# Optimization experiments

Measured on AMD Instinct MI355X. Metric: run time of the kernel, lower is better.

Reference implementation:

```python
import jax, jax.numpy as jnp
import numpy as np
from jax import lax

N, C, H, W = 64, 96, 18, 32
S_IN = 320          # input_state_size
HEADS, HD = 4, 96 // 4
HID = 96            # HIDDEN_SIZE
ENC = 320           # ENC_SIZE
K = 3               # KERNEL_SIZE


def _conv(x, k, b):
    y = lax.conv_general_dilated(x, k, (1, 1), 'SAME',
                                 dimension_numbers=('NCHW', 'OIHW', 'NCHW'))
    return y + b[None, :, None, None]


def setup_inputs() -> dict:
    key = jax.random.key(0)
    ks = jax.random.split(key, 16)
    sc = 0.02
    inp = {
        'x': jax.random.normal(ks[0], (N, C, H, W), jnp.float32),
        'x_state': jax.random.normal(ks[1], (N, S_IN), jnp.float32),
        'actor_keys': jax.random.randint(ks[2], (N,), 0, N),
        'hidden_states': 0.1 * jax.random.normal(ks[3], (N, HID, H, W), jnp.float32),
        # modulation Linear(S_IN -> 2*C), bias init 0
        'W_mod': sc * jax.random.normal(ks[4], (S_IN, 2 * C), jnp.float32),
        'b_mod': jnp.zeros((2 * C,), jnp.float32),
        # FiLM attention: qkv 1x1 proj and output proj
        'W_qkv': sc * jax.random.normal(ks[5], (C, 3 * C), jnp.float32),
        'b_qkv': jnp.zeros((3 * C,), jnp.float32),
        'W_proj': sc * jax.random.normal(ks[6], (C, C), jnp.float32),
        'b_proj': jnp.zeros((C,), jnp.float32),
        # IRConv2dCell (ConvGRU-style): gates conv (2C -> 2*HID), candidate conv (2C -> HID)
        'K_zr': sc * jax.random.normal(ks[7], (2 * HID, 2 * C, K, K), jnp.float32),
        'b_zr': jnp.zeros((2 * HID,), jnp.float32),
        'K_c': sc * jax.random.normal(ks[8], (HID, 2 * C, K, K), jnp.float32),
        'b_c': jnp.zeros((HID,), jnp.float32),
        # PosConv: learned positional map + 1x1 conv to ENC
        'pos_emb': sc * jax.random.normal(ks[9], (1, HID, H, W), jnp.float32),
        'W_pos': sc * jax.random.normal(ks[10], (ENC, HID), jnp.float32),
        'b_pos': jnp.zeros((ENC,), jnp.float32),
    }
    return inp


def reference(x, x_state, actor_keys, hidden_states,
              W_mod, b_mod, W_qkv, b_qkv, W_proj, b_proj,
              K_zr, b_zr, K_c, b_c, pos_emb, W_pos, b_pos):
    HW = H * W
    # modulation -> FiLM params
    mod = x_state @ W_mod + b_mod                       # [N, 2C]
    mm, mb = jnp.split(mod, 2, axis=1)                  # [N, C] each
    # FiLM-conditioned attention over spatial positions
    xm = x * mm[:, :, None, None] + mb[:, :, None, None]  # [N,C,H,W]
    xf = xm.reshape(N, C, HW).transpose(0, 2, 1)          # [N,HW,C]
    qkv = xf @ W_qkv + b_qkv                              # [N,HW,3C]
    q, k, v = jnp.split(qkv, 3, axis=-1)
    q = q.reshape(N, HW, HEADS, HD).transpose(0, 2, 1, 3)  # [N,h,HW,hd]
    k = k.reshape(N, HW, HEADS, HD).transpose(0, 2, 1, 3)
    v = v.reshape(N, HW, HEADS, HD).transpose(0, 2, 1, 3)
    attn = jax.nn.softmax(jnp.einsum('nhqd,nhkd->nhqk', q, k) / np.sqrt(HD), axis=-1)
    o = jnp.einsum('nhqk,nhkd->nhqd', attn, v)            # [N,h,HW,hd]
    o = o.transpose(0, 2, 1, 3).reshape(N, HW, C)
    o = o @ W_proj + b_proj
    y = x + o.transpose(0, 2, 1).reshape(N, C, H, W)      # residual
    # actor-keyed recurrent conv memory cell (gather per actor key)
    h = hidden_states[actor_keys]                         # [N,HID,H,W]
    xh = jnp.concatenate([y, h], axis=1)                  # [N,2C,H,W]
    zr = _conv(xh, K_zr, b_zr)
    z, r = jnp.split(jax.nn.sigmoid(zr), 2, axis=1)
    c = jnp.tanh(_conv(jnp.concatenate([y, r * h], axis=1), K_c, b_c))
    h_new = (1.0 - z) * h + z * c                         # [N,HID,H,W]
    # pooled outputs
    x_visual = h_new.reshape(N, HID, H // 2, 2, W // 2, 2).mean(axis=(3, 5))
    e = h_new + pos_emb
    enc = jnp.einsum('nchw,oc->nohw', e, W_pos) + b_pos[None, :, None, None]
    x_visual_enc = enc.max(axis=(2, 3))                   # [N,ENC]
    return (x_visual, x_visual_enc)
```

## Files before the change

kernel.cpp:

```cpp
#include <hip/hip_runtime.h>
#include <hip/hip_bf16.h>
#include <math.h>

#define NN 64
#define CC 96
#define HH 18
#define WW 32
#define HWP 576
#define SIN 320
#define NHEADS 4
#define HDIM 24
#define HIDC 96
#define ENCC 320

#define MOD_OFF   0
#define A_OFF     12288
#define Y_OFF     (A_OFF)
#define Z_OFF     (A_OFF + 3538944)
#define RH_OFF    (A_OFF + 7077888)
#define O_OFF     (A_OFF + 10616832)
#define HN_OFF    (O_OFF)
#define PART_OFF  (O_OFF + 3538944)
#define WTZR_OFF  (PART_OFF + 163840)
#define WTC_OFF   (WTZR_OFF + 165888)

typedef __attribute__((ext_vector_type(8))) short short8;
typedef __attribute__((ext_vector_type(4))) float f32x4;
typedef __attribute__((ext_vector_type(2))) unsigned int uint2v;
#define MFMA16(a, b, c) __builtin_amdgcn_mfma_f32_16x16x32_bf16(a, b, c, 0, 0, 0)

__device__ inline unsigned short f2bf(float f) {
  __hip_bfloat16 h = __float2bfloat16(f);
  return *reinterpret_cast<unsigned short*>(&h);
}
__device__ inline unsigned int cvtpk(float lo, float hi) {
  unsigned int r;
  asm volatile("v_cvt_pk_bf16_f32 %0, %1, %2" : "=v"(r) : "v"(lo), "v"(hi));
  return r;
}
union S8U { short8 s; unsigned int u[4]; };

__global__ __launch_bounds__(192) void k_mod(const float* __restrict__ xs,
    const float* __restrict__ Wm, const float* __restrict__ bm,
    float* __restrict__ mod) {
  __shared__ float s[SIN];
  int n = blockIdx.x;
  for (int i = threadIdx.x; i < SIN; i += 192) s[i] = xs[n * SIN + i];
  __syncthreads();
  int j = threadIdx.x;
  float acc = bm[j];
  #pragma unroll 4
  for (int k = 0; k < SIN; ++k) acc = fmaf(s[k], Wm[k * 192 + j], acc);
  mod[n * 192 + j] = acc;
}

__global__ __launch_bounds__(256) void k_qkv(const float* __restrict__ x,
    const float* __restrict__ mod, const float* __restrict__ Wq,
    const float* __restrict__ bq, float* __restrict__ qkv) {
  int id = blockIdx.x;
  int n = id & 63, pt = id >> 6;
  int p0 = pt * 96;
  __shared__ __align__(16) short XT[96 * 104];
  int tid = threadIdx.x, lane = tid & 63, wid = tid >> 6;
  int wr = wid >> 1, wcn = wid & 1;
  int cl = lane & 15, kg = lane >> 4;
  #pragma unroll
  for (int w = 0; w < 9; ++w) {
    int lin = tid + 256 * w;
    int cp = lin / 48, pp = (lin % 48) * 2;
    float mA = mod[n * 192 + 2 * cp], bA = mod[n * 192 + 96 + 2 * cp];
    float mB = mod[n * 192 + 2 * cp + 1], bB = mod[n * 192 + 96 + 2 * cp + 1];
    float2 xa = *reinterpret_cast<const float2*>(
        &x[((size_t)n * CC + 2 * cp) * HWP + p0 + pp]);
    float2 xb = *reinterpret_cast<const float2*>(
        &x[((size_t)n * CC + 2 * cp + 1) * HWP + p0 + pp]);
    *reinterpret_cast<unsigned int*>(&XT[pp * 104 + 2 * cp]) =
        cvtpk(fmaf(xa.x, mA, bA), fmaf(xb.x, mB, bB));
    *reinterpret_cast<unsigned int*>(&XT[(pp + 1) * 104 + 2 * cp]) =
        cvtpk(fmaf(xa.y, mA, bA), fmaf(xb.y, mB, bB));
  }
  __syncthreads();

  f32x4 acc[3][9];
  #pragma unroll
  for (int mt = 0; mt < 3; ++mt)
    #pragma unroll
    for (int nt = 0; nt < 9; ++nt) acc[mt][nt] = (f32x4){0.f, 0.f, 0.f, 0.f};

  #pragma unroll
  for (int kc = 0; kc < 3; ++kc) {
    short8 af[3];
    #pragma unroll
    for (int mt = 0; mt < 3; ++mt) {
      int row = wr * 48 + mt * 16 + cl;
      af[mt] = *reinterpret_cast<const short8*>(
          &XT[row * 104 + kc * 32 + kg * 8]);
    }
    #pragma unroll
    for (int nt = 0; nt < 9; ++nt) {
      int j = wcn * 144 + nt * 16 + cl;
      const float* wp = Wq + (size_t)(kc * 32 + kg * 8) * 288 + j;
      S8U b;
      b.u[0] = cvtpk(wp[0], wp[288]);
      b.u[1] = cvtpk(wp[576], wp[864]);
      b.u[2] = cvtpk(wp[1152], wp[1440]);
      b.u[3] = cvtpk(wp[1728], wp[2016]);
      #pragma unroll
      for (int mt = 0; mt < 3; ++mt)
        acc[mt][nt] = MFMA16(af[mt], b.s, acc[mt][nt]);
    }
  }

  #pragma unroll
  for (int nt = 0; nt < 9; ++nt) {
    int j = wcn * 144 + nt * 16 + cl;
    float bias = bq[j];
    #pragma unroll
    for (int mt = 0; mt < 3; ++mt) {
      int pr = p0 + wr * 48 + mt * 16 + kg * 4;
      float* dst = qkv + ((size_t)n * HWP + pr) * 288 + j;
      dst[0] = acc[mt][nt][0] + bias;
      dst[288] = acc[mt][nt][1] + bias;
      dst[576] = acc[mt][nt][2] + bias;
      dst[864] = acc[mt][nt][3] + bias;
    }
  }
}

__global__ __launch_bounds__(256) void k_attn(const float* __restrict__ qkv,
                                              float* __restrict__ o) {
  int id = blockIdx.x;
  int n = id & 63, head = id >> 6;
  __shared__ __align__(16) short K_lds[576 * 40];
  __shared__ __align__(16) short VT_lds[24 * 584];
  __shared__ __align__(16) short P_lds[4 * 144 * 40];
  int tid = threadIdx.x, lane = tid & 63, wid = tid >> 6;
  int cl = lane & 15, kg = lane >> 4;
  const float* base = qkv + (size_t)n * HWP * 288;
  int qoff = head * HDIM, koff = CC + head * HDIM, voff = 2 * CC + head * HDIM;
  const float scale = 0.2041241452319315f;

  for (int p = tid; p < HWP; p += 256) {
    const float* ksrc = base + (size_t)p * 288 + koff;
    #pragma unroll
    for (int g = 0; g < 3; ++g) {
      float4 a = *(const float4*)(ksrc + g * 8);
      float4 b = *(const float4*)(ksrc + g * 8 + 4);
      S8U t;
      t.u[0] = cvtpk(a.x, a.y); t.u[1] = cvtpk(a.z, a.w);
      t.u[2] = cvtpk(b.x, b.y); t.u[3] = cvtpk(b.z, b.w);
      *reinterpret_cast<short8*>(&K_lds[p * 40 + g * 8]) = t.s;
    }
    *reinterpret_cast<short8*>(&K_lds[p * 40 + 24]) =
        (short8){0, 0, 0, 0, 0, 0, 0, 0};
    const float* vsrc = base + (size_t)p * 288 + voff;
    #pragma unroll
    for (int d = 0; d < HDIM; ++d) VT_lds[d * 584 + p] = (short)f2bf(vsrc[d]);
  }

  int qbase = wid * 144;
  short8 qf[9];
  #pragma unroll
  for (int qt = 0; qt < 9; ++qt) {
    if (kg < 3) {
      const float* qs =
          base + (size_t)(qbase + qt * 16 + cl) * 288 + qoff + kg * 8;
      float4 a = *(const float4*)qs;
      float4 b = *(const float4*)(qs + 4);
      S8U t;
      t.u[0] = cvtpk(a.x * scale, a.y * scale);
      t.u[1] = cvtpk(a.z * scale, a.w * scale);
      t.u[2] = cvtpk(b.x * scale, b.y * scale);
      t.u[3] = cvtpk(b.z * scale, b.w * scale);
      qf[qt] = t.s;
    } else {
      qf[qt] = (short8){0, 0, 0, 0, 0, 0, 0, 0};
    }
  }
  __syncthreads();

  f32x4 acc[9][2];
  float m[9], l[9];
  #pragma unroll
  for (int qt = 0; qt < 9; ++qt) {
    acc[qt][0] = (f32x4){0.f, 0.f, 0.f, 0.f};
    acc[qt][1] = (f32x4){0.f, 0.f, 0.f, 0.f};
    m[qt] = -1e30f; l[qt] = 0.f;
  }
  short* pw = P_lds + wid * 5760;
  const f32x4 z4 = (f32x4){0.f, 0.f, 0.f, 0.f};

  for (int ch = 0; ch < 18; ++ch) {
    int key0 = ch * 32;
    short8 ka0 = *reinterpret_cast<const short8*>(
        &K_lds[(key0 + cl) * 40 + kg * 8]);
    short8 ka1 = *reinterpret_cast<const short8*>(
        &K_lds[(key0 + 16 + cl) * 40 + kg * 8]);
    #pragma unroll
    for (int qt = 0; qt < 9; ++qt) {
      f32x4 s0 = MFMA16(ka0, qf[qt], z4);
      f32x4 s1 = MFMA16(ka1, qf[qt], z4);
      float mx = fmaxf(fmaxf(fmaxf(s0[0], s0[1]), fmaxf(s0[2], s0[3])),
                       fmaxf(fmaxf(s1[0], s1[1]), fmaxf(s1[2], s1[3])));
      mx = fmaxf(mx, __shfl_xor(mx, 16));
      mx = fmaxf(mx, __shfl_xor(mx, 32));
      float mn = fmaxf(m[qt], mx);
      float corr = __expf(m[qt] - mn);
      float p0 = __expf(s0[0] - mn), p1 = __expf(s0[1] - mn);
      float p2 = __expf(s0[2] - mn), p3 = __expf(s0[3] - mn);
      float p4 = __expf(s1[0] - mn), p5 = __expf(s1[1] - mn);
      float p6 = __expf(s1[2] - mn), p7 = __expf(s1[3] - mn);
      float sum = ((p0 + p1) + (p2 + p3)) + ((p4 + p5) + (p6 + p7));
      sum += __shfl_xor(sum, 16);
      sum += __shfl_xor(sum, 32);
      l[qt] = l[qt] * corr + sum;
      m[qt] = mn;
      float c0 = __shfl(corr, kg * 4 + 0);
      float c1 = __shfl(corr, kg * 4 + 1);
      float c2 = __shfl(corr, kg * 4 + 2);
      float c3 = __shfl(corr, kg * 4 + 3);
      acc[qt][0][0] *= c0; acc[qt][0][1] *= c1;
      acc[qt][0][2] *= c2; acc[qt][0][3] *= c3;
      acc[qt][1][0] *= c0; acc[qt][1][1] *= c1;
      acc[qt][1][2] *= c2; acc[qt][1][3] *= c3;
      uint2v w0 = {cvtpk(p0, p1), cvtpk(p2, p3)};
      uint2v w1 = {cvtpk(p4, p5), cvtpk(p6, p7)};
      short* prow = pw + (qt * 16 + cl) * 40;
      *reinterpret_cast<uint2v*>(&prow[4 * kg]) = w0;
      *reinterpret_cast<uint2v*>(&prow[16 + 4 * kg]) = w1;
    }
    short8 vb0 = *reinterpret_cast<const short8*>(
        &VT_lds[cl * 584 + key0 + kg * 8]);
    short8 vb1 = (cl < 8) ? *reinterpret_cast<const short8*>(
                                &VT_lds[(16 + cl) * 584 + key0 + kg * 8])
                          : (short8){0, 0, 0, 0, 0, 0, 0, 0};
    #pragma unroll
    for (int qt = 0; qt < 9; ++qt) {
      short8 pa = *reinterpret_cast<const short8*>(
          &pw[(qt * 16 + cl) * 40 + kg * 8]);
      acc[qt][0] = MFMA16(pa, vb0, acc[qt][0]);
      acc[qt][1] = MFMA16(pa, vb1, acc[qt][1]);
    }
  }

  #pragma unroll
  for (int qt = 0; qt < 9; ++qt) {
    float li0 = 1.f / __shfl(l[qt], kg * 4 + 0);
    float li1 = 1.f / __shfl(l[qt], kg * 4 + 1);
    float li2 = 1.f / __shfl(l[qt], kg * 4 + 2);
    float li3 = 1.f / __shfl(l[qt], kg * 4 + 3);
    #pragma unroll
    for (int dt = 0; dt < 2; ++dt) {
      int d = dt * 16 + cl;
      if (dt == 1 && cl >= 8) continue;
      size_t ob = ((size_t)n * HWP + qbase + qt * 16 + kg * 4) * CC
                  + head * HDIM + d;
      o[ob] = acc[qt][dt][0] * li0;
      o[ob + CC] = acc[qt][dt][1] * li1;
      o[ob + 2 * CC] = acc[qt][dt][2] * li2;
      o[ob + 3 * CC] = acc[qt][dt][3] * li3;
    }
  }
}

__global__ __launch_bounds__(256) void k_proj(const float* __restrict__ o,
    const float* __restrict__ Wp, const float* __restrict__ bp,
    const float* __restrict__ x, float* __restrict__ y) {
  int id = blockIdx.x;
  int n = id & 63, pt = id >> 6;
  int p0 = pt * 96;
  __shared__ __align__(16) short XT[96 * 104];
  int tid = threadIdx.x, lane = tid & 63, wid = tid >> 6;
  int wr = wid >> 1, wcn = wid & 1;
  int cl = lane & 15, kg = lane >> 4;
  #pragma unroll
  for (int w = 0; w < 9; ++w) {
    int lin = tid + 256 * w;
    int p = lin / 24, cg = lin % 24;
    float4 v = *reinterpret_cast<const float4*>(
        &o[((size_t)n * HWP + p0 + p) * CC + cg * 4]);
    uint2v u = {cvtpk(v.x, v.y), cvtpk(v.z, v.w)};
    *reinterpret_cast<uint2v*>(&XT[p * 104 + cg * 4]) = u;
  }
  __syncthreads();

  f32x4 acc[3][3];
  #pragma unroll
  for (int mt = 0; mt < 3; ++mt)
    #pragma unroll
    for (int nt = 0; nt < 3; ++nt) acc[mt][nt] = (f32x4){0.f, 0.f, 0.f, 0.f};

  #pragma unroll
  for (int kc = 0; kc < 3; ++kc) {
    short8 af[3];
    #pragma unroll
    for (int mt = 0; mt < 3; ++mt) {
      int row = wr * 48 + mt * 16 + cl;
      af[mt] = *reinterpret_cast<const short8*>(
          &XT[row * 104 + kc * 32 + kg * 8]);
    }
    #pragma unroll
    for (int nt = 0; nt < 3; ++nt) {
      int j = wcn * 48 + nt * 16 + cl;
      const float* wp = Wp + (size_t)(kc * 32 + kg * 8) * 96 + j;
      S8U b;
      b.u[0] = cvtpk(wp[0], wp[96]);
      b.u[1] = cvtpk(wp[192], wp[288]);
      b.u[2] = cvtpk(wp[384], wp[480]);
      b.u[3] = cvtpk(wp[576], wp[672]);
      #pragma unroll
      for (int mt = 0; mt < 3; ++mt)
        acc[mt][nt] = MFMA16(af[mt], b.s, acc[mt][nt]);
    }
  }

  #pragma unroll
  for (int nt = 0; nt < 3; ++nt) {
    int j = wcn * 48 + nt * 16 + cl;
    float bias = bp[j];
    #pragma unroll
    for (int mt = 0; mt < 3; ++mt) {
      int pr = p0 + wr * 48 + mt * 16 + kg * 4;
      size_t yi = ((size_t)n * CC + j) * HWP + pr;
      float4 xv = *reinterpret_cast<const float4*>(&x[yi]);
      float4 o4 = {xv.x + acc[mt][nt][0] + bias, xv.y + acc[mt][nt][1] + bias,
                   xv.z + acc[mt][nt][2] + bias, xv.w + acc[mt][nt][3] + bias};
      *reinterpret_cast<float4*>(&y[yi]) = o4;
    }
  }
}

__global__ __launch_bounds__(256) void k_wt(const float* __restrict__ Kzr,
    const float* __restrict__ Kc, short* __restrict__ wz,
    short* __restrict__ wc) {
  int idx = blockIdx.x * 256 + threadIdx.x;
  if (idx < 36864) {
    int oc = idx / 192, ic = idx % 192;
    const float* s = Kzr + (size_t)idx * 9;
    #pragma unroll
    for (int t = 0; t < 9; ++t)
      wz[(t * 192 + oc) * 192 + ic] = (short)f2bf(s[t]);
  } else {
    int j = idx - 36864;
    if (j < 18432) {
      int oc = j / 192, ic = j % 192;
      const float* s = Kc + (size_t)j * 9;
      #pragma unroll
      for (int t = 0; t < 9; ++t)
        wc[(t * 96 + oc) * 192 + ic] = (short)f2bf(s[t]);
    }
  }
}


__global__ __launch_bounds__(256) void k_conv_zr(const float* __restrict__ y,
    const float* __restrict__ hidden, const int* __restrict__ keys,
    const short* __restrict__ wt, const float* __restrict__ bb,
    float* __restrict__ z, float* __restrict__ rh) {
  int id = blockIdx.x;
  int n = id & 63, b = id >> 6;
  int bp = b % 6, bo = b / 6;
  int key = keys[n];
  int ocb = bo * 96;
  __shared__ __align__(16) short XT[170 * 200];
  int tid = threadIdx.x;
  int lane = tid & 63, wid = tid >> 6;
  int wr = wid >> 1, wc = wid & 1;
  int col = lane & 15, kg = lane >> 4;
  int icp = tid >> 4, psub = tid & 15;
  int pb = psub * 10;
  int pg0 = (3 * bp - 1) * 32;
  unsigned int* XTu = reinterpret_cast<unsigned int*>(XT);

  for (int i = tid; i < 17000; i += 256) XTu[i] = 0;

  f32x4 acc[3][3];
  #pragma unroll
  for (int m = 0; m < 3; ++m)
    #pragma unroll
    for (int nt = 0; nt < 3; ++nt) acc[m][nt] = (f32x4){0.f, 0.f, 0.f, 0.f};
  int rowm[3], pxm[3];
  #pragma unroll
  for (int m = 0; m < 3; ++m) {
    int pl = wr * 48 + m * 16 + col;
    rowm[m] = pl >> 5;
    pxm[m] = pl & 31;
  }
  int wl = (ocb + wc * 48 + col) * 192 + kg * 8;
  const float* hsrc = hidden + (size_t)key * HIDC * HWP;
  __syncthreads();

  #pragma unroll
  for (int c = 0; c < 6; ++c) {
    const float* s0 = (c < 3)
        ? y + ((size_t)n * CC + c * 32 + 2 * icp) * HWP
        : hsrc + (size_t)((c - 3) * 32 + 2 * icp) * HWP;
    const float* s1 = s0 + HWP;
    #pragma unroll
    for (int j = 0; j < 5; ++j) {
      int pos = pb + 2 * j;
      int pg = pg0 + pos;
      bool ok = (pg >= 0 && pg < HWP);
      float2 a = ok ? *reinterpret_cast<const float2*>(s0 + pg)
                    : float2{0.f, 0.f};
      float2 bv = ok ? *reinterpret_cast<const float2*>(s1 + pg)
                     : float2{0.f, 0.f};
      int pidx0 = (pos >> 5) * 34 + 1 + (pos & 31);
      int pidx1 = ((pos + 1) >> 5) * 34 + 1 + ((pos + 1) & 31);
      XTu[pidx0 * 100 + c * 16 + icp] = cvtpk(a.x, bv.x);
      XTu[pidx1 * 100 + c * 16 + icp] = cvtpk(a.y, bv.y);
    }
  }
  __syncthreads();

  for (int t = 0; t < 9; ++t) {
    int dyp = t / 3, dxp = t % 3;
    const short* wci = wt + wl + t * 36864;
    #pragma unroll
    for (int q = 0; q < 6; ++q) {
      short8 b0 = *reinterpret_cast<const short8*>(wci + q * 32);
      short8 b1 = *reinterpret_cast<const short8*>(wci + q * 32 + 3072);
      short8 b2 = *reinterpret_cast<const short8*>(wci + q * 32 + 6144);
      #pragma unroll
      for (int m = 0; m < 3; ++m) {
        int pidx = (rowm[m] + dyp) * 34 + pxm[m] + dxp;
        short8 a = *reinterpret_cast<const short8*>(
            XT + pidx * 200 + q * 32 + kg * 8);
        acc[m][0] = MFMA16(a, b0, acc[m][0]);
        acc[m][1] = MFMA16(a, b1, acc[m][1]);
        acc[m][2] = MFMA16(a, b2, acc[m][2]);
      }
    }
  }

  #pragma unroll
  for (int nt = 0; nt < 3; ++nt) {
    int oc = ocb + wc * 48 + nt * 16 + col;
    float bias = bb[oc];
    #pragma unroll
    for (int m = 0; m < 3; ++m) {
      int p0 = bp * 96 + wr * 48 + m * 16 + kg * 4;
      f32x4 v = acc[m][nt];
      float e0 = 1.f / (1.f + __expf(-(v[0] + bias)));
      float e1 = 1.f / (1.f + __expf(-(v[1] + bias)));
      float e2 = 1.f / (1.f + __expf(-(v[2] + bias)));
      float e3 = 1.f / (1.f + __expf(-(v[3] + bias)));
      if (oc < CC) {
        float4 o4 = {e0, e1, e2, e3};
        *reinterpret_cast<float4*>(&z[((size_t)n * CC + oc) * HWP + p0]) = o4;
      } else {
        int c2 = oc - CC;
        float4 h4 = *reinterpret_cast<const float4*>(
            &hidden[((size_t)key * HIDC + c2) * HWP + p0]);
        float4 o4 = {e0 * h4.x, e1 * h4.y, e2 * h4.z, e3 * h4.w};
        *reinterpret_cast<float4*>(&rh[((size_t)n * CC + c2) * HWP + p0]) = o4;
      }
    }
  }
}

__global__ __launch_bounds__(256) void k_conv_c(const float* __restrict__ y,
    const float* __restrict__ rh, const int* __restrict__ keys,
    const float* __restrict__ z, const float* __restrict__ hidden,
    const short* __restrict__ wt, const float* __restrict__ bb,
    float* __restrict__ hn) {
  int id = blockIdx.x;
  int n = id & 63, bp = id >> 6;
  int key = keys[n];
  __shared__ __align__(16) short XT[170 * 200];
  int tid = threadIdx.x;
  int lane = tid & 63, wid = tid >> 6;
  int wr = wid >> 1, wc = wid & 1;
  int col = lane & 15, kg = lane >> 4;
  int icp = tid >> 4, psub = tid & 15;
  int pb = psub * 10;
  int pg0 = (3 * bp - 1) * 32;
  unsigned int* XTu = reinterpret_cast<unsigned int*>(XT);

  for (int i = tid; i < 17000; i += 256) XTu[i] = 0;

  f32x4 acc[3][3];
  #pragma unroll
  for (int m = 0; m < 3; ++m)
    #pragma unroll
    for (int nt = 0; nt < 3; ++nt) acc[m][nt] = (f32x4){0.f, 0.f, 0.f, 0.f};
  int rowm[3], pxm[3];
  #pragma unroll
  for (int m = 0; m < 3; ++m) {
    int pl = wr * 48 + m * 16 + col;
    rowm[m] = pl >> 5;
    pxm[m] = pl & 31;
  }
  int wl = (wc * 48 + col) * 192 + kg * 8;
  const float* rsrc = rh + (size_t)n * CC * HWP;
  __syncthreads();

  #pragma unroll
  for (int c = 0; c < 6; ++c) {
    const float* s0 = (c < 3)
        ? y + ((size_t)n * CC + c * 32 + 2 * icp) * HWP
        : rsrc + (size_t)((c - 3) * 32 + 2 * icp) * HWP;
    const float* s1 = s0 + HWP;
    #pragma unroll
    for (int j = 0; j < 5; ++j) {
      int pos = pb + 2 * j;
      int pg = pg0 + pos;
      bool ok = (pg >= 0 && pg < HWP);
      float2 a = ok ? *reinterpret_cast<const float2*>(s0 + pg)
                    : float2{0.f, 0.f};
      float2 bv = ok ? *reinterpret_cast<const float2*>(s1 + pg)
                     : float2{0.f, 0.f};
      int pidx0 = (pos >> 5) * 34 + 1 + (pos & 31);
      int pidx1 = ((pos + 1) >> 5) * 34 + 1 + ((pos + 1) & 31);
      XTu[pidx0 * 100 + c * 16 + icp] = cvtpk(a.x, bv.x);
      XTu[pidx1 * 100 + c * 16 + icp] = cvtpk(a.y, bv.y);
    }
  }
  __syncthreads();

  for (int t = 0; t < 9; ++t) {
    int dyp = t / 3, dxp = t % 3;
    const short* wci = wt + wl + t * 18432;
    #pragma unroll
    for (int q = 0; q < 6; ++q) {
      short8 b0 = *reinterpret_cast<const short8*>(wci + q * 32);
      short8 b1 = *reinterpret_cast<const short8*>(wci + q * 32 + 3072);
      short8 b2 = *reinterpret_cast<const short8*>(wci + q * 32 + 6144);
      #pragma unroll
      for (int m = 0; m < 3; ++m) {
        int pidx = (rowm[m] + dyp) * 34 + pxm[m] + dxp;
        short8 a = *reinterpret_cast<const short8*>(
            XT + pidx * 200 + q * 32 + kg * 8);
        acc[m][0] = MFMA16(a, b0, acc[m][0]);
        acc[m][1] = MFMA16(a, b1, acc[m][1]);
        acc[m][2] = MFMA16(a, b2, acc[m][2]);
      }
    }
  }

  #pragma unroll
  for (int nt = 0; nt < 3; ++nt) {
    int oc = wc * 48 + nt * 16 + col;
    float bias = bb[oc];
    #pragma unroll
    for (int m = 0; m < 3; ++m) {
      int p0 = bp * 96 + wr * 48 + m * 16 + kg * 4;
      f32x4 v = acc[m][nt];
      float c0 = tanhf(v[0] + bias);
      float c1 = tanhf(v[1] + bias);
      float c2v = tanhf(v[2] + bias);
      float c3 = tanhf(v[3] + bias);
      float4 z4 = *reinterpret_cast<const float4*>(
          &z[((size_t)n * CC + oc) * HWP + p0]);
      float4 h4 = *reinterpret_cast<const float4*>(
          &hidden[((size_t)key * HIDC + oc) * HWP + p0]);
      float4 o4 = {(1.f - z4.x) * h4.x + z4.x * c0,
                   (1.f - z4.y) * h4.y + z4.y * c1,
                   (1.f - z4.z) * h4.z + z4.z * c2v,
                   (1.f - z4.w) * h4.w + z4.w * c3};
      *reinterpret_cast<float4*>(&hn[((size_t)n * CC + oc) * HWP + p0]) = o4;
    }
  }
}

__global__ void k_pool(const float* __restrict__ hn, float* __restrict__ out) {
  int idx = blockIdx.x * 256 + threadIdx.x;
  if (idx >= NN * CC * 9 * 16) return;
  int j = idx & 15, i = (idx >> 4) % 9, nc = idx / 144;
  const float* b = hn + (size_t)nc * HWP + (2 * i) * WW + 2 * j;
  out[idx] = 0.25f * (b[0] + b[1] + b[WW] + b[WW + 1]);
}

__global__ __launch_bounds__(256) void k_enc(const float* __restrict__ hn,
    const float* __restrict__ pos, const float* __restrict__ Wp,
    float* __restrict__ part) {
  int id = blockIdx.x;
  int n = id & 63, pt = id >> 6;
  int p0 = pt * 96;
  __shared__ __align__(16) short XT[96 * 104];
  int tid = threadIdx.x, lane = tid & 63, wid = tid >> 6;
  int wr = wid >> 1, wcn = wid & 1;
  int cl = lane & 15, kg = lane >> 4;
  #pragma unroll
  for (int w = 0; w < 9; ++w) {
    int lin = tid + 256 * w;
    int cp = lin / 48, pp = (lin % 48) * 2;
    float2 ha = *reinterpret_cast<const float2*>(
        &hn[((size_t)n * CC + 2 * cp) * HWP + p0 + pp]);
    float2 hb = *reinterpret_cast<const float2*>(
        &hn[((size_t)n * CC + 2 * cp + 1) * HWP + p0 + pp]);
    float2 pa = *reinterpret_cast<const float2*>(&pos[(2 * cp) * HWP + p0 + pp]);
    float2 pc = *reinterpret_cast<const float2*>(
        &pos[(2 * cp + 1) * HWP + p0 + pp]);
    *reinterpret_cast<unsigned int*>(&XT[pp * 104 + 2 * cp]) =
        cvtpk(ha.x + pa.x, hb.x + pc.x);
    *reinterpret_cast<unsigned int*>(&XT[(pp + 1) * 104 + 2 * cp]) =
        cvtpk(ha.y + pa.y, hb.y + pc.y);
  }
  __syncthreads();

  f32x4 acc[3][10];
  #pragma unroll
  for (int mt = 0; mt < 3; ++mt)
    #pragma unroll
    for (int nt = 0; nt < 10; ++nt) acc[mt][nt] = (f32x4){0.f, 0.f, 0.f, 0.f};

  #pragma unroll
  for (int kc = 0; kc < 3; ++kc) {
    short8 af[3];
    #pragma unroll
    for (int mt = 0; mt < 3; ++mt) {
      int row = wr * 48 + mt * 16 + cl;
      af[mt] = *reinterpret_cast<const short8*>(
          &XT[row * 104 + kc * 32 + kg * 8]);
    }
    #pragma unroll
    for (int nt = 0; nt < 10; ++nt) {
      int oc = wcn * 160 + nt * 16 + cl;
      const float* wp = Wp + (size_t)oc * CC + kc * 32 + kg * 8;
      float4 w0 = *reinterpret_cast<const float4*>(wp);
      float4 w1 = *reinterpret_cast<const float4*>(wp + 4);
      S8U b;
      b.u[0] = cvtpk(w0.x, w0.y); b.u[1] = cvtpk(w0.z, w0.w);
      b.u[2] = cvtpk(w1.x, w1.y); b.u[3] = cvtpk(w1.z, w1.w);
      #pragma unroll
      for (int mt = 0; mt < 3; ++mt)
        acc[mt][nt] = MFMA16(af[mt], b.s, acc[mt][nt]);
    }
  }

  #pragma unroll
  for (int nt = 0; nt < 10; ++nt) {
    float mx = -1e30f;
    #pragma unroll
    for (int mt = 0; mt < 3; ++mt) {
      mx = fmaxf(mx, fmaxf(fmaxf(acc[mt][nt][0], acc[mt][nt][1]),
                           fmaxf(acc[mt][nt][2], acc[mt][nt][3])));
    }
    mx = fmaxf(mx, __shfl_xor(mx, 16));
    mx = fmaxf(mx, __shfl_xor(mx, 32));
    if (kg == 0) {
      int oc = wcn * 160 + nt * 16 + cl;
      part[(((size_t)n * 6 + pt) * 2 + wr) * ENCC + oc] = mx;
    }
  }
}

__global__ __launch_bounds__(320) void k_reduce(const float* __restrict__ part,
    const float* __restrict__ bpos, float* __restrict__ out) {
  int n = blockIdx.x, o = threadIdx.x;
  float mx = -1e30f;
  #pragma unroll
  for (int t = 0; t < 12; ++t)
    mx = fmaxf(mx, part[((size_t)n * 12 + t) * ENCC + o]);
  out[NN * CC * 144 + n * ENCC + o] = mx + bpos[o];
}

extern "C" void kernel_launch(void* const* d_in, const int* in_sizes, int n_in,
                              void* d_out, int out_size, void* d_ws, size_t ws_size,
                              hipStream_t stream) {
  const float* x       = (const float*)d_in[0];
  const float* x_state = (const float*)d_in[1];
  const int*   keys    = (const int*)d_in[2];
  const float* hidden  = (const float*)d_in[3];
  const float* W_mod   = (const float*)d_in[4];
  const float* b_mod   = (const float*)d_in[5];
  const float* W_qkv   = (const float*)d_in[6];
  const float* b_qkv   = (const float*)d_in[7];
  const float* W_proj  = (const float*)d_in[8];
  const float* b_proj  = (const float*)d_in[9];
  const float* K_zr    = (const float*)d_in[10];
  const float* b_zr    = (const float*)d_in[11];
  const float* K_c     = (const float*)d_in[12];
  const float* b_c     = (const float*)d_in[13];
  const float* pos_emb = (const float*)d_in[14];
  const float* W_pos   = (const float*)d_in[15];
  const float* b_pos   = (const float*)d_in[16];
  float* out = (float*)d_out;
  float* ws  = (float*)d_ws;
  short* wtzr = (short*)(ws + WTZR_OFF);
  short* wtc  = (short*)(ws + WTC_OFF);

  k_wt<<<216, 256, 0, stream>>>(K_zr, K_c, wtzr, wtc);
  k_mod<<<NN, 192, 0, stream>>>(x_state, W_mod, b_mod, ws + MOD_OFF);
  k_qkv<<<384, 256, 0, stream>>>(x, ws + MOD_OFF, W_qkv, b_qkv, ws + A_OFF);
  k_attn<<<256, 256, 0, stream>>>(ws + A_OFF, ws + O_OFF);
  k_proj<<<384, 256, 0, stream>>>(ws + O_OFF, W_proj, b_proj, x, ws + Y_OFF);
  k_conv_zr<<<768, 256, 0, stream>>>(ws + Y_OFF, hidden, keys, wtzr, b_zr,
                                     ws + Z_OFF, ws + RH_OFF);
  k_conv_c<<<384, 256, 0, stream>>>(ws + Y_OFF, ws + RH_OFF, keys, ws + Z_OFF,
                                    hidden, wtc, b_c, ws + HN_OFF);
  k_pool<<<3456, 256, 0, stream>>>(ws + HN_OFF, out);
  k_enc<<<384, 256, 0, stream>>>(ws + HN_OFF, pos_emb, W_pos, ws + PART_OFF);
  k_reduce<<<NN, 320, 0, stream>>>(ws + PART_OFF, b_pos, out);
}
```

Measured before the change: 314.8 us.

## Fuse weight prep into mod kernel, pool into enc, coalesce conv staging loads

Merges the weight-transpose kernel into the FiLM modulation kernel and folds the 2x2 average pool into the encoder kernel, removing two launches. The conv kernels now stage input so that adjacent threads read adjacent pixel pairs, giving coalesced global loads instead of a 10-pixel stride per thread. They also partially unroll the tap loop by three. The pool work inside k_enc lengthens that kernel and the unroll may raise register pressure.

```diff
diff --git a/kernel.cpp b/kernel.cpp
--- a/kernel.cpp
+++ b/kernel.cpp
@@ -40,18 +40,43 @@
 }
 union S8U { short8 s; unsigned int u[4]; };
 
-__global__ __launch_bounds__(192) void k_mod(const float* __restrict__ xs,
+__global__ __launch_bounds__(256) void k_modwt(const float* __restrict__ xs,
     const float* __restrict__ Wm, const float* __restrict__ bm,
-    float* __restrict__ mod) {
+    float* __restrict__ mod, const float* __restrict__ Kzr,
+    const float* __restrict__ Kc, short* __restrict__ wz,
+    short* __restrict__ wc) {
   __shared__ float s[SIN];
-  int n = blockIdx.x;
-  for (int i = threadIdx.x; i < SIN; i += 192) s[i] = xs[n * SIN + i];
-  __syncthreads();
-  int j = threadIdx.x;
-  float acc = bm[j];
-  #pragma unroll 4
-  for (int k = 0; k < SIN; ++k) acc = fmaf(s[k], Wm[k * 192 + j], acc);
-  mod[n * 192 + j] = acc;
+  int bid = blockIdx.x;
+  if (bid < 64) {
+    int n = bid;
+    for (int i = threadIdx.x; i < SIN; i += 256) s[i] = xs[n * SIN + i];
+    __syncthreads();
+    int j = threadIdx.x;
+    if (j < 192) {
+      float acc = bm[j];
+      #pragma unroll 4
+      for (int k = 0; k < SIN; ++k) acc = fmaf(s[k], Wm[k * 192 + j], acc);
+      mod[n * 192 + j] = acc;
+    }
+  } else {
+    int idx = (bid - 64) * 256 + threadIdx.x;
+    if (idx < 36864) {
+      int oc = idx / 192, ic = idx % 192;
+      const float* src = Kzr + (size_t)idx * 9;
+      #pragma unroll
+      for (int t = 0; t < 9; ++t)
+        wz[(t * 192 + oc) * 192 + ic] = (short)f2bf(src[t]);
+    } else {
+      int j = idx - 36864;
+      if (j < 18432) {
+        int oc = j / 192, ic = j % 192;
+        const float* src = Kc + (size_t)j * 9;
+        #pragma unroll
+        for (int t = 0; t < 9; ++t)
+          wc[(t * 96 + oc) * 192 + ic] = (short)f2bf(src[t]);
+      }
+    }
+  }
 }
 
 __global__ __launch_bounds__(256) void k_qkv(const float* __restrict__ x,
@@ -330,28 +355,6 @@
   }
 }
 
-__global__ __launch_bounds__(256) void k_wt(const float* __restrict__ Kzr,
-    const float* __restrict__ Kc, short* __restrict__ wz,
-    short* __restrict__ wc) {
-  int idx = blockIdx.x * 256 + threadIdx.x;
-  if (idx < 36864) {
-    int oc = idx / 192, ic = idx % 192;
-    const float* s = Kzr + (size_t)idx * 9;
-    #pragma unroll
-    for (int t = 0; t < 9; ++t)
-      wz[(t * 192 + oc) * 192 + ic] = (short)f2bf(s[t]);
-  } else {
-    int j = idx - 36864;
-    if (j < 18432) {
-      int oc = j / 192, ic = j % 192;
-      const float* s = Kc + (size_t)j * 9;
-      #pragma unroll
-      for (int t = 0; t < 9; ++t)
-        wc[(t * 96 + oc) * 192 + ic] = (short)f2bf(s[t]);
-    }
-  }
-}
-
 
 __global__ __launch_bounds__(256) void k_conv_zr(const float* __restrict__ y,
     const float* __restrict__ hidden, const int* __restrict__ keys,
@@ -368,7 +371,6 @@
   int wr = wid >> 1, wc = wid & 1;
   int col = lane & 15, kg = lane >> 4;
   int icp = tid >> 4, psub = tid & 15;
-  int pb = psub * 10;
   int pg0 = (3 * bp - 1) * 32;
   unsigned int* XTu = reinterpret_cast<unsigned int*>(XT);
 
@@ -398,7 +400,7 @@
     const float* s1 = s0 + HWP;
     #pragma unroll
     for (int j = 0; j < 5; ++j) {
-      int pos = pb + 2 * j;
+      int pos = 32 * j + 2 * psub;
       int pg = pg0 + pos;
       bool ok = (pg >= 0 && pg < HWP);
       float2 a = ok ? *reinterpret_cast<const float2*>(s0 + pg)
@@ -406,13 +408,13 @@
       float2 bv = ok ? *reinterpret_cast<const float2*>(s1 + pg)
                      : float2{0.f, 0.f};
       int pidx0 = (pos >> 5) * 34 + 1 + (pos & 31);
-      int pidx1 = ((pos + 1) >> 5) * 34 + 1 + ((pos + 1) & 31);
       XTu[pidx0 * 100 + c * 16 + icp] = cvtpk(a.x, bv.x);
-      XTu[pidx1 * 100 + c * 16 + icp] = cvtpk(a.y, bv.y);
-    }
-  }
-  __syncthreads();
-
+      XTu[(pidx0 + 1) * 100 + c * 16 + icp] = cvtpk(a.y, bv.y);
+    }
+  }
+  __syncthreads();
+
+  #pragma unroll 3
   for (int t = 0; t < 9; ++t) {
     int dyp = t / 3, dxp = t % 3;
     const short* wci = wt + wl + t * 36864;
@@ -473,7 +475,6 @@
   int wr = wid >> 1, wc = wid & 1;
   int col = lane & 15, kg = lane >> 4;
   int icp = tid >> 4, psub = tid & 15;
-  int pb = psub * 10;
   int pg0 = (3 * bp - 1) * 32;
   unsigned int* XTu = reinterpret_cast<unsigned int*>(XT);
 
@@ -503,7 +504,7 @@
     const float* s1 = s0 + HWP;
     #pragma unroll
     for (int j = 0; j < 5; ++j) {
-      int pos = pb + 2 * j;
+      int pos = 32 * j + 2 * psub;
       int pg = pg0 + pos;
       bool ok = (pg >= 0 && pg < HWP);
       float2 a = ok ? *reinterpret_cast<const float2*>(s0 + pg)
@@ -511,13 +512,13 @@
       float2 bv = ok ? *reinterpret_cast<const float2*>(s1 + pg)
                      : float2{0.f, 0.f};
       int pidx0 = (pos >> 5) * 34 + 1 + (pos & 31);
-      int pidx1 = ((pos + 1) >> 5) * 34 + 1 + ((pos + 1) & 31);
       XTu[pidx0 * 100 + c * 16 + icp] = cvtpk(a.x, bv.x);
-      XTu[pidx1 * 100 + c * 16 + icp] = cvtpk(a.y, bv.y);
-    }
-  }
-  __syncthreads();
-
+      XTu[(pidx0 + 1) * 100 + c * 16 + icp] = cvtpk(a.y, bv.y);
+    }
+  }
+  __syncthreads();
+
+  #pragma unroll 3
   for (int t = 0; t < 9; ++t) {
     int dyp = t / 3, dxp = t % 3;
     const short* wci = wt + wl + t * 18432;
@@ -563,17 +564,9 @@
   }
 }
 
-__global__ void k_pool(const float* __restrict__ hn, float* __restrict__ out) {
-  int idx = blockIdx.x * 256 + threadIdx.x;
-  if (idx >= NN * CC * 9 * 16) return;
-  int j = idx & 15, i = (idx >> 4) % 9, nc = idx / 144;
-  const float* b = hn + (size_t)nc * HWP + (2 * i) * WW + 2 * j;
-  out[idx] = 0.25f * (b[0] + b[1] + b[WW] + b[WW + 1]);
-}
-
 __global__ __launch_bounds__(256) void k_enc(const float* __restrict__ hn,
     const float* __restrict__ pos, const float* __restrict__ Wp,
-    float* __restrict__ part) {
+    float* __restrict__ part, float* __restrict__ out) {
   int id = blockIdx.x;
   int n = id & 63, pt = id >> 6;
   int p0 = pt * 96;
@@ -581,6 +574,15 @@
   int tid = threadIdx.x, lane = tid & 63, wid = tid >> 6;
   int wr = wid >> 1, wcn = wid & 1;
   int cl = lane & 15, kg = lane >> 4;
+
+  #pragma unroll
+  for (int r = 0; r < 9; ++r) {
+    int idx = id * 2304 + r * 256 + tid;
+    int jj = idx & 15, ii = (idx >> 4) % 9, nc = idx / 144;
+    const float* bsrc = hn + (size_t)nc * HWP + (2 * ii) * WW + 2 * jj;
+    out[idx] = 0.25f * (bsrc[0] + bsrc[1] + bsrc[WW] + bsrc[WW + 1]);
+  }
+
   #pragma unroll
   for (int w = 0; w < 9; ++w) {
     int lin = tid + 256 * w;
@@ -681,8 +683,8 @@
   short* wtzr = (short*)(ws + WTZR_OFF);
   short* wtc  = (short*)(ws + WTC_OFF);
 
-  k_wt<<<216, 256, 0, stream>>>(K_zr, K_c, wtzr, wtc);
-  k_mod<<<NN, 192, 0, stream>>>(x_state, W_mod, b_mod, ws + MOD_OFF);
+  k_modwt<<<280, 256, 0, stream>>>(x_state, W_mod, b_mod, ws + MOD_OFF,
+                                   K_zr, K_c, wtzr, wtc);
   k_qkv<<<384, 256, 0, stream>>>(x, ws + MOD_OFF, W_qkv, b_qkv, ws + A_OFF);
   k_attn<<<256, 256, 0, stream>>>(ws + A_OFF, ws + O_OFF);
   k_proj<<<384, 256, 0, stream>>>(ws + O_OFF, W_proj, b_proj, x, ws + Y_OFF);
@@ -690,7 +692,7 @@
                                      ws + Z_OFF, ws + RH_OFF);
   k_conv_c<<<384, 256, 0, stream>>>(ws + Y_OFF, ws + RH_OFF, keys, ws + Z_OFF,
                                     hidden, wtc, b_c, ws + HN_OFF);
-  k_pool<<<3456, 256, 0, stream>>>(ws + HN_OFF, out);
-  k_enc<<<384, 256, 0, stream>>>(ws + HN_OFF, pos_emb, W_pos, ws + PART_OFF);
+  k_enc<<<384, 256, 0, stream>>>(ws + HN_OFF, pos_emb, W_pos, ws + PART_OFF,
+                                 out);
   k_reduce<<<NN, 320, 0, stream>>>(ws + PART_OFF, b_pos, out);
 }
```

Result: slower. 322.4 us (+2.4%).
